# Kernel optimization log

Hardware: AMD Instinct MI355X
Metric: run time of the kernel (lower is better)

The kernel has to match this reference:

```python
import jax, jax.numpy as jnp
import numpy as np

# ---- model dims (match torch para_dict) ----
B, F1, F2, F_OUT = 16, 32, 64, 10
B0, B1, B2 = 32, 16, 8           # bandwidths: input / layer1 / layer2
M1, M2 = 2 * B1 - 1, 2 * B2 - 1  # padded spectral width over signed m
NUM_POINTS = 1
EPS = 1e-5

_LF = np.concatenate([[0.0], np.cumsum(np.log(np.arange(1.0, 200.0)))])  # _LF[i] = log(i!)

def _betas(b):
    return np.pi * (2.0 * np.arange(2 * b) + 1.0) / (4.0 * b)

def _quad_weights(b):
    # Driscoll-Healy quadrature weights on the 2b beta grid
    beta = _betas(b)
    k = np.arange(b)[:, None]
    s = np.sum(np.sin((2 * k + 1) * beta[None, :]) / (2 * k + 1), axis=0)
    return (2.0 / b) * np.sin(beta) * s

def _wig(l, m, n, betas):
    # small Wigner d^l_{m,n}(beta), vectorized over betas (float64)
    kmin, kmax = max(0, m - n), min(l + m, l - n)
    k = np.arange(kmin, kmax + 1)
    pref = 0.5 * (_LF[l + m] + _LF[l - m] + _LF[l + n] + _LF[l - n])
    coef = (-1.0) ** k * np.exp(pref - _LF[k] - _LF[l + m - k] - _LF[l - n - k] - _LF[n - m + k])
    cb, sb = np.cos(betas / 2)[:, None], np.sin(betas / 2)[:, None]
    return (coef * cb ** (2 * l + m - n - 2 * k) * sb ** (n - m + 2 * k)).sum(1)

def _build():
    b0g, b1g, b2g = _betas(B0), _betas(B1), _betas(B2)
    w0, w1q = _quad_weights(B0), _quad_weights(B1)
    d1f = np.zeros((B1, 2 * B0, M1))        # S2 forward: w_j * d^l_{m0}(beta_j)
    d1i = np.zeros((B1, 2 * B1, M1, M1))    # SO3 inverse at layer-1 grid, * (2l+1)
    d2f = np.zeros((B2, 2 * B1, M2, M2))    # SO3 forward at layer-1 grid, * w_j
    d2i = np.zeros((B2, 2 * B2, M2, M2))    # SO3 inverse at layer-2 grid, * (2l+1)
    mask1, mask2 = np.zeros((B1, M1)), np.zeros((B2, M2, M2))
    for l in range(B1):
        o = (B1 - 1) - l
        mask1[l, o:o + 2 * l + 1] = 1.0
        for m in range(-l, l + 1):
            d1f[l, :, o + m + l] = w0 * _wig(l, m, 0, b0g)
            for n in range(-l, l + 1):
                d1i[l, :, o + m + l, o + n + l] = (2 * l + 1) * _wig(l, m, n, b1g)
    for l in range(B2):
        o = (B2 - 1) - l
        mask2[l, o:o + 2 * l + 1, o:o + 2 * l + 1] = 1.0
        for m in range(-l, l + 1):
            for n in range(-l, l + 1):
                d2f[l, :, o + m + l, o + n + l] = w1q * _wig(l, m, n, b1g)
                d2i[l, :, o + m + l, o + n + l] = (2 * l + 1) * _wig(l, m, n, b2g)
    return d1f, d1i, d2f, d2i, mask1, mask2

_d1f, _d1i, _d2f, _d2i, _m1, _m2 = _build()
D1F = jnp.asarray(_d1f, jnp.float32)
D1I = jnp.asarray(_d1i, jnp.float32)
D2F = jnp.asarray(_d2f, jnp.float32)
D2I = jnp.asarray(_d2i, jnp.float32)
MASK1 = jnp.asarray(_m1, jnp.float32)
MASK2 = jnp.asarray(_m2, jnp.float32)
IDX1 = jnp.asarray(np.arange(-(B1 - 1), B1) % (2 * B0), jnp.int32)
IDXG1 = jnp.asarray(np.arange(-(B1 - 1), B1) % (2 * B1), jnp.int32)
IDX2 = jnp.asarray(np.arange(-(B2 - 1), B2) % (2 * B1), jnp.int32)
IDXG2 = jnp.asarray(np.arange(-(B2 - 1), B2) % (2 * B2), jnp.int32)

def _so3_ifft(yh, d_inv, idx, n):
    # yh: [B,F,L,M,M] SO3 spectrum -> signal [B,F,2b,2b,2b] on (beta, alpha, gamma)
    f = jnp.einsum('ljmn,bflmn->bfjmn', d_inv, yh)
    z = jnp.zeros(f.shape[:3] + (n, n), dtype=f.dtype)
    z = z.at[..., idx[:, None], idx[None, :]].set(f)
    return jnp.real(jnp.fft.ifft2(z, axes=(-2, -1))) * (n * n)

def _forward(x, w1r, w1i, w2r, w2i, conv3_w, conv3_b, bn_gamma, bn_beta, fc_w, fc_b):
    # ---- S2 convolution (b_in=B0 -> b_out=B1) ----
    xm = jnp.take(jnp.fft.fft(x, axis=-1), IDX1, axis=-1)      # alpha FFT, signed m  [B,1,2B0,M1]
    xh = jnp.einsum('ljm,bcjm->bclm', D1F, xm)                 # S2 FFT  [B,1,B1,M1]
    w1 = (w1r + 1j * w1i) * MASK1                              # [1,F1,B1,M1]
    yh1 = jnp.einsum('bclm,cfln->bflmn', xh, jnp.conj(w1))     # outer product -> SO3 spectrum
    r1 = jax.nn.relu(_so3_ifft(yh1, D1I, IDXG1, 2 * B1))       # [B,F1,2B1,2B1,2B1]
    # ---- SO3 convolution (b_in=B1 -> b_out=B2) ----
    xf2 = jnp.fft.fft2(r1, axes=(-2, -1))                      # over (alpha, gamma)
    xmn = xf2[..., IDX2[:, None], IDX2[None, :]]               # [B,F1,2B1,M2,M2]
    xh2 = jnp.einsum('ljmn,bcjmn->bclmn', D2F, xmn)            # SO3 FFT [B,F1,B2,M2,M2]
    w2 = (w2r + 1j * w2i) * MASK2                              # [F1,F2,B2,M2,M2]
    yh2 = jnp.einsum('bclmk,cflnk->bflmn', xh2, jnp.conj(w2))  # x_hat @ w_hat^H per l
    r2 = jax.nn.relu(_so3_ifft(yh2, D2I, IDXG2, 2 * B2))       # [B,F2,2B2,2B2,2B2]
    # ---- head: conv1d -> relu -> batchnorm(train) -> linear ----
    feat = r2[:, :, 0, 0, 0].reshape(B, 1, NUM_POINTS * F2)
    c3 = jax.lax.conv_general_dilated(feat, conv3_w, (1,), 'VALID',
                                      dimension_numbers=('NCH', 'OIH', 'NCH'))
    r3 = jax.nn.relu(c3 + conv3_b[None, :, None])              # [B,10,57]
    mu = jnp.mean(r3, axis=(0, 2), keepdims=True)
    var = jnp.mean((r3 - mu) ** 2, axis=(0, 2), keepdims=True)
    bn = bn_gamma[None, :, None] * (r3 - mu) * jax.lax.rsqrt(var + EPS) + bn_beta[None, :, None]
    return bn.reshape(B, -1) @ fc_w.T + fc_b

def setup_inputs():
    key = jax.random.key(0)
    ks = jax.random.split(key, 8)
    f = jnp.float32
    return {
        "x": jax.random.normal(ks[0], (B, 1, 2 * B0, 2 * B0), f),
        "w1r": 0.1 * jax.random.normal(ks[1], (1, F1, B1, M1), f),
        "w1i": 0.1 * jax.random.normal(ks[2], (1, F1, B1, M1), f),
        "w2r": 0.05 * jax.random.normal(ks[3], (F1, F2, B2, M2, M2), f),
        "w2i": 0.05 * jax.random.normal(ks[4], (F1, F2, B2, M2, M2), f),
        "conv3_w": 0.3 * jax.random.normal(ks[5], (10, 1, 8), f),
        "conv3_b": jnp.zeros((10,), f),
        "bn_gamma": jnp.ones((10,), f),
        "bn_beta": jnp.zeros((10,), f),
        "fc_w": 0.05 * jax.random.normal(ks[6], (F_OUT, 10 * (NUM_POINTS * F2 - 8 + 1)), f),
        "fc_b": jnp.zeros((F_OUT,), f),
    }

def reference(x, w1r, w1i, w2r, w2i, conv3_w, conv3_b, bn_gamma, bn_beta, fc_w, fc_b):
    return _forward(x, w1r, w1i, w2r, w2i, conv3_w, conv3_b, bn_gamma, bn_beta, fc_w, fc_b)
```

## Files before the change

kernel.cpp:

```cpp
#include <hip/hip_runtime.h>
#include <math.h>

#ifndef M_PI
#define M_PI 3.14159265358979323846
#endif

#define OFF_TRIG 708
#define OFF_D1F 900
#define OFF_D1I 32644
#define OFF_D2F 540548
#define OFF_S2  598148
#define OFF_XH  599948
#define OFF_XMN 615820
#define OFF_U   7988620
#define OFF_FEAT 9831820

static __device__ __forceinline__ int iabs_(int v) { return v < 0 ? -v : v; }

static __device__ __forceinline__ double powi_d(double x, int e) {
    double r = 1.0;
    while (e) { if (e & 1) r *= x; x *= x; e >>= 1; }
    return r;
}

__global__ __launch_bounds__(256) void k0a_tables(float* __restrict__ ws) {
    double* T = (double*)ws;
    int t = threadIdx.x;
    __shared__ double lg[64];
    if (t < 64) lg[t] = (t == 0) ? 0.0 : log((double)t);
    __syncthreads();
    if (t == 0) {
        double s = 0.0;
        for (int i = 0; i < 64; ++i) { s += lg[i]; T[i] = s; }
    }
    if (t < 64) {
        double beta = M_PI * (2.0 * t + 1.0) / 128.0;
        double s = 0.0;
        for (int k = 0; k < 32; ++k) s += sin((2.0 * k + 1.0) * beta) / (2.0 * k + 1.0);
        T[64 + t] = 2.0 / 32.0 * sin(beta) * s;
        T[160 + t] = cos(0.5 * beta);
        T[224 + t] = sin(0.5 * beta);
    }
    if (t >= 64 && t < 96) {
        int j = t - 64;
        double beta = M_PI * (2.0 * j + 1.0) / 64.0;
        double s = 0.0;
        for (int k = 0; k < 16; ++k) s += sin((2.0 * k + 1.0) * beta) / (2.0 * k + 1.0);
        T[128 + j] = 2.0 / 16.0 * sin(beta) * s;
        T[288 + j] = cos(0.5 * beta);
        T[320 + j] = sin(0.5 * beta);
    }
    if (t == 96) {
        T[352] = cos(M_PI / 64.0);
        T[353] = sin(M_PI / 64.0);
    }
    float2* F = (float2*)(ws + OFF_TRIG);
    if (t < 32) {
        double a = 2.0 * M_PI * (double)t / 32.0;
        F[t] = make_float2((float)cos(a), (float)sin(a));
    }
    if (t >= 128 && t < 192) {
        int i = t - 128;
        double a = 2.0 * M_PI * (double)i / 64.0;
        F[32 + i] = make_float2((float)cos(a), (float)sin(a));
    }
    for (int i = t; i < 1024; i += 256) ws[OFF_FEAT + i] = 0.f;
}

__device__ double wig_fast(int l, int m, int n, double cb, double sb, const double* LF) {
    int kmin = max(0, m - n), kmax = min(l + m, l - n);
    if (kmax < kmin) return 0.0;
    double lc = 0.5 * (LF[l + m] + LF[l - m] + LF[l + n] + LF[l - n])
              - LF[kmin] - LF[l + m - kmin] - LF[l - n - kmin] - LF[n - m + kmin];
    double t = exp(lc) * powi_d(cb, 2 * l + m - n - 2 * kmin)
                       * powi_d(sb, n - m + 2 * kmin);
    if (kmin & 1) t = -t;
    double ratio = (sb * sb) / (cb * cb);
    double s = t;
    for (int k = kmin; k < kmax; ++k) {
        t *= -(((double)(l + m - k) * (double)(l - n - k)) /
               ((double)(k + 1) * (double)(n - m + k + 1))) * ratio;
        s += t;
    }
    return s;
}

__global__ __launch_bounds__(256) void k0_consts(float* __restrict__ ws) {
    const double* T = (const double*)ws;
    __shared__ double LF[64];
    int tid = threadIdx.x;
    if (tid < 64) LF[tid] = T[tid];
    __syncthreads();
    int gid = blockIdx.x * 256 + tid;
    if (gid >= 599048) return;

    if (gid < 31744) {
        int mh = gid % 31, j = (gid / 31) % 64, l = gid / (31 * 64);
        int m = mh - 15;
        double v = 0.0;
        if (iabs_(m) <= l)
            v = T[64 + j] * wig_fast(l, m, 0, T[160 + j], T[224 + j], LF);
        ws[OFF_D1F + gid] = (float)v;
    } else if (gid < 539648) {
        int r = gid - 31744;
        int nh = r & 31;
        int l  = (r >> 5) & 15;
        int mh = (r >> 9) % 31;
        int j  = r / (512 * 31);
        int m = mh - 15, n = nh - 15;
        double v = 0.0;
        if (nh < 31 && iabs_(m) <= l && iabs_(n) <= l)
            v = (2.0 * l + 1.0) * wig_fast(l, m, n, T[288 + j], T[320 + j], LF);
        ws[OFF_D1I + r] = (float)v;
    } else if (gid < 597248) {
        int r = gid - 539648;
        int l = r & 7;
        int pq = (r >> 3) % 225;
        int j = r / 1800;
        int mh = pq / 15, nh = pq % 15;
        int m = mh - 7, n = nh - 7;
        double v = 0.0;
        if (iabs_(m) <= l && iabs_(n) <= l)
            v = T[128 + j] * wig_fast(l, m, n, T[288 + j], T[320 + j], LF);
        ws[OFF_D2F + r] = (float)v;
    } else {
        int r = gid - 597248;
        int nh = r % 15, mh = (r / 15) % 15, l = r / 225;
        int m = mh - 7, n = nh - 7;
        double v = 0.0;
        if (iabs_(m) <= l && iabs_(n) <= l)
            v = (2.0 * l + 1.0) * wig_fast(l, m, n, T[352], T[353], LF);
        ws[OFF_S2 + r] = (float)v;
    }
}

__global__ __launch_bounds__(256) void k1_xh(const float* __restrict__ x,
                                             const float* __restrict__ ws,
                                             float2* __restrict__ xh) {
    __shared__ float  xs[64 * 64];
    __shared__ float2 xm[64 * 8];
    __shared__ float2 cs64[64];
    int c = blockIdx.x, b = blockIdx.y, tid = threadIdx.x;
    int mh0 = c * 8;
    int cnt = min(8, 31 - mh0);
    for (int i = tid; i < 4096; i += 256) xs[i] = x[b * 4096 + i];
    if (tid < 64) cs64[tid] = ((const float2*)(ws + OFF_TRIG))[32 + tid];
    __syncthreads();
    for (int i = tid; i < 512; i += 256) {
        int j = i >> 3, mi = i & 7;
        if (mi < cnt) {
            int mu = mh0 + mi - 15;
            float re = 0.f, im = 0.f;
            for (int t = 0; t < 64; ++t) {
                float2 w = cs64[(mu * t) & 63];
                float xv = xs[j * 64 + t];
                re += xv * w.x;
                im -= xv * w.y;
            }
            xm[i] = make_float2(re, im);
        }
    }
    __syncthreads();
    const float* D1F = ws + OFF_D1F;
    if (tid < 128) {
        int l = tid >> 3, mi = tid & 7;
        if (mi < cnt) {
            int mh = mh0 + mi;
            float re = 0.f, im = 0.f;
            for (int j = 0; j < 64; ++j) {
                float d = D1F[(l * 64 + j) * 31 + mh];
                float2 v = xm[j * 8 + mi];
                re += d * v.x;
                im += d * v.y;
            }
            xh[b * 496 + l * 31 + mh] = make_float2(re, im);
        }
    }
}

__global__ __launch_bounds__(256) void k2_planes(const float* __restrict__ w1r,
                                                 const float* __restrict__ w1i,
                                                 const float* __restrict__ ws,
                                                 float2* __restrict__ xmn) {
    __shared__ char ar[16896];
    __shared__ float2 cs[32];
    float2* As  = (float2*)ar;
    float2* Wc  = (float2*)(ar + 4096);
    float2* f1  = (float2*)(ar + 8448);
    float2* fH  = (float2*)ar;
    float2* tls = (float2*)(ar + 4608);
    float*  ssb = (float*)(ar + 9216);
    float2* gg  = (float2*)ar;

    int j = blockIdx.x, f = blockIdx.y, b = blockIdx.z;
    int tid = threadIdx.x;
    const float2* xh = (const float2*)(ws + OFF_XH);

    if (tid < 32) cs[tid] = ((const float2*)(ws + OFF_TRIG))[tid];
    for (int i = tid; i < 496; i += 256) As[i] = xh[b * 496 + i];
    for (int i = tid; i < 512; i += 256) {
        int l = i >> 5, nh = i & 31;
        float mask = (nh < 31 && iabs_(nh - 15) <= l) ? 1.0f : 0.0f;
        int src = f * 496 + l * 31 + min(nh, 30);
        Wc[i] = make_float2(w1r[src] * mask, -w1i[src] * mask);
    }
    __syncthreads();
    {
        int mrow = tid >> 3;
        int nh0 = (tid & 7) * 4;
        if (mrow < 31) {
            int l0 = iabs_(mrow - 15);
            float2 a0 = {0,0}, a1 = {0,0}, a2 = {0,0}, a3 = {0,0};
            const float* Dbase = ws + OFF_D1I + ((j * 31 + mrow) * 16) * 32 + nh0;
            for (int l = l0; l < 16; ++l) {
                float2 a = As[l * 31 + mrow];
                float4 w01 = *(const float4*)(Wc + l * 32 + nh0);
                float4 w23 = *(const float4*)(Wc + l * 32 + nh0 + 2);
                float4 d = *(const float4*)(Dbase + l * 32);
                float t;
                t = a.x*w01.x - a.y*w01.y; a0.x += d.x*t;
                t = a.x*w01.y + a.y*w01.x; a0.y += d.x*t;
                t = a.x*w01.z - a.y*w01.w; a1.x += d.y*t;
                t = a.x*w01.w + a.y*w01.z; a1.y += d.y*t;
                t = a.x*w23.x - a.y*w23.y; a2.x += d.z*t;
                t = a.x*w23.y + a.y*w23.x; a2.y += d.z*t;
                t = a.x*w23.z - a.y*w23.w; a3.x += d.w*t;
                t = a.x*w23.w + a.y*w23.z; a3.y += d.w*t;
            }
            float2* fr = f1 + mrow * 34 + nh0;
            fr[0] = a0; fr[1] = a1; fr[2] = a2; fr[3] = a3;
        }
    }
    __syncthreads();
    for (int i = tid; i < 512; i += 256) {
        int mm = i >> 5, nh = i & 31;
        float2 v = make_float2(0.f, 0.f);
        if (nh < 31) {
            float2 a = f1[(mm + 15) * 34 + nh];
            float2 bb = f1[(15 - mm) * 34 + (30 - nh)];
            v = make_float2(0.5f * (a.x + bb.x), 0.5f * (a.y - bb.y));
        }
        fH[mm * 34 + nh] = v;
    }
    __syncthreads();
    if (tid < 128) {
        int mm = tid >> 3, v0 = tid & 7;
        const float2* frow = fH + mm * 34;
        float2 a0 = {0,0}, a1 = {0,0}, a2 = {0,0}, a3 = {0,0};
        for (int nb = 0; nb < 32; nb += 4) {
            float4 q01 = *(const float4*)(frow + nb);
            float4 q23 = *(const float4*)(frow + nb + 2);
            {
                float2 w = cs[((nb - 15) * v0) & 31];
                float px = q01.x*w.x - q01.y*w.y, py = q01.x*w.y + q01.y*w.x;
                a0.x += px; a0.y += py;  a1.x -= py; a1.y += px;
                a2.x -= px; a2.y -= py;  a3.x += py; a3.y -= px;
            }
            {
                float2 w = cs[((nb - 14) * v0) & 31];
                float px = q01.z*w.x - q01.w*w.y, py = q01.z*w.y + q01.w*w.x;
                a0.x += px; a0.y += py;  a1.x -= px; a1.y -= py;
                a2.x += px; a2.y += py;  a3.x -= px; a3.y -= py;
            }
            {
                float2 w = cs[((nb - 13) * v0) & 31];
                float px = q23.x*w.x - q23.y*w.y, py = q23.x*w.y + q23.y*w.x;
                a0.x += px; a0.y += py;  a1.x += py; a1.y -= px;
                a2.x -= px; a2.y -= py;  a3.x -= py; a3.y += px;
            }
            {
                float2 w = cs[((nb - 12) * v0) & 31];
                float px = q23.z*w.x - q23.w*w.y, py = q23.z*w.y + q23.w*w.x;
                a0.x += px; a0.y += py;  a1.x += px; a1.y += py;
                a2.x += px; a2.y += py;  a3.x += px; a3.y += py;
            }
        }
        float2* trow = tls + mm * 33;
        trow[v0] = a0; trow[v0 + 8] = a1; trow[v0 + 16] = a2; trow[v0 + 24] = a3;
    } else if (tid < 161) {
        tls[16 * 33 + (tid - 128)] = make_float2(0.f, 0.f);
    }
    __syncthreads();
    {
        int v = tid & 31, u0 = tid >> 5;
        float s0 = 0, s1 = 0, s2 = 0, s3 = 0;
        for (int mb = 0; mb < 4; ++mb) {
            int r1 = mb * 4 + 1;
            {
                float2 tv = tls[r1 * 33 + v];       float2 w = cs[(r1 * u0) & 31];
                float qx = tv.x*w.x - tv.y*w.y, qy = tv.x*w.y + tv.y*w.x;
                s0 += qx; s1 -= qy; s2 -= qx; s3 += qy;
            }
            {
                float2 tv = tls[(r1 + 1) * 33 + v]; float2 w = cs[((r1 + 1) * u0) & 31];
                float qx = tv.x*w.x - tv.y*w.y;
                s0 += qx; s1 -= qx; s2 += qx; s3 -= qx;
            }
            {
                float2 tv = tls[(r1 + 2) * 33 + v]; float2 w = cs[((r1 + 2) * u0) & 31];
                float qx = tv.x*w.x - tv.y*w.y, qy = tv.x*w.y + tv.y*w.x;
                s0 += qx; s1 += qy; s2 -= qx; s3 -= qy;
            }
            {
                float2 tv = tls[(r1 + 3) * 33 + v]; float2 w = cs[((r1 + 3) * u0) & 31];
                float qx = tv.x*w.x - tv.y*w.y;
                s0 += qx; s1 += qx; s2 += qx; s3 += qx;
            }
        }
        float t0x = tls[v].x;
        ssb[u0 * 33 + v]        = fmaxf(t0x + 2.f * s0, 0.f);
        ssb[(u0 + 8) * 33 + v]  = fmaxf(t0x + 2.f * s1, 0.f);
        ssb[(u0 + 16) * 33 + v] = fmaxf(t0x + 2.f * s2, 0.f);
        ssb[(u0 + 24) * 33 + v] = fmaxf(t0x + 2.f * s3, 0.f);
    }
    __syncthreads();
    {
        int u = tid >> 3, q = tid & 7;
        int qm = q & 3;
        float r1 = (qm == 0) ? 1.f : (qm == 2 ? -1.f : 0.f);
        float r2 = (qm & 1) ? -1.f : 1.f;
        float i1 = (qm == 1) ? -1.f : (qm == 3 ? 1.f : 0.f);
        float gx = 0.f, gy = 0.f;
        const float* srow = ssb + u * 33;
        for (int vb = 0; vb < 8; ++vb) {
            float s0 = srow[vb], s1 = srow[vb + 8], s2 = srow[vb + 16], s3 = srow[vb + 24];
            float zre = s0 + r1 * s1 + r2 * s2 + r1 * s3;
            float zim = i1 * (s1 - s3);
            float2 w = cs[(q * vb) & 31];
            gx += zre * w.x + zim * w.y;
            gy += zim * w.x - zre * w.y;
        }
        gg[u * 15 + 7 + q] = make_float2(gx, gy);
        if (q) gg[u * 15 + 7 - q] = make_float2(gx, -gy);
    }
    __syncthreads();
    if (tid < 113) {
        int ph, qh;
        if (tid < 105) { ph = 8 + tid / 15; qh = tid % 15; }
        else           { ph = 7; qh = 7 + (tid - 105); }
        int p = ph - 7;
        float hx = 0.f, hy = 0.f;
        for (int u = 0; u < 32; ++u) {
            float2 gv = gg[u * 15 + qh];
            float2 w = cs[(-(p * u)) & 31];
            hx += gv.x * w.x - gv.y * w.y;
            hy += gv.x * w.y + gv.y * w.x;
        }
        float2* outp = xmn + ((size_t)((b * 32 + f) * 32 + j)) * 225;
        outp[ph * 15 + qh] = make_float2(hx, hy);
        if (ph > 7 || qh > 7)
            outp[(14 - ph) * 15 + (14 - qh)] = make_float2(hx, -hy);
    }
}

__global__ __launch_bounds__(256) void k34_U(const float* __restrict__ ws,
                                             const float2* __restrict__ xmn,
                                             float2* __restrict__ U) {
    __shared__ float2 xh2s[1800];
    __shared__ float  S2s[1800];
    int bc = blockIdx.x, tid = threadIdx.x;

    for (int i = tid; i < 1800; i += 256) S2s[i] = ws[OFF_S2 + i];

    float2 acc[8];
#pragma unroll
    for (int l = 0; l < 8; ++l) acc[l] = make_float2(0.f, 0.f);
    if (tid < 225) {
        const float2* xp = xmn + (size_t)bc * 7200;
        const float4* dw = (const float4*)(ws + OFF_D2F);
        for (int j = 0; j < 32; ++j) {
            float2 xv = xp[j * 225 + tid];
            float4 dA = dw[(j * 225 + tid) * 2];
            float4 dB = dw[(j * 225 + tid) * 2 + 1];
            acc[0].x += dA.x * xv.x; acc[0].y += dA.x * xv.y;
            acc[1].x += dA.y * xv.x; acc[1].y += dA.y * xv.y;
            acc[2].x += dA.z * xv.x; acc[2].y += dA.z * xv.y;
            acc[3].x += dA.w * xv.x; acc[3].y += dA.w * xv.y;
            acc[4].x += dB.x * xv.x; acc[4].y += dB.x * xv.y;
            acc[5].x += dB.y * xv.x; acc[5].y += dB.y * xv.y;
            acc[6].x += dB.z * xv.x; acc[6].y += dB.z * xv.y;
            acc[7].x += dB.w * xv.x; acc[7].y += dB.w * xv.y;
        }
#pragma unroll
        for (int l = 0; l < 8; ++l) xh2s[l * 225 + tid] = acc[l];
    }
    __syncthreads();

    for (int idx = tid; idx < 1800; idx += 256) {
        int l = idx / 225;
        int rem = idx - l * 225;
        int n = rem / 15, k = rem - n * 15;
        float2 a = make_float2(0.f, 0.f);
        for (int m = 0; m < 15; ++m) {
            float s = S2s[(l * 15 + m) * 15 + n];
            float2 v = xh2s[l * 225 + m * 15 + k];
            a.x += s * v.x;
            a.y += s * v.y;
        }
        U[(size_t)bc * 1800 + idx] = a;
    }
}

__global__ __launch_bounds__(256) void k5_feat(const float* __restrict__ w2r,
                                               const float* __restrict__ w2i,
                                               const float2* __restrict__ U,
                                               float* __restrict__ feat) {
    __shared__ char ar[57600];
    float2* Us  = (float2*)ar;
    float2* Wsh = (float2*)(ar + 28800);
    int bx = blockIdx.x;
    int c = bx >> 5, l = (bx >> 2) & 7, fc = bx & 3;
    int tid = threadIdx.x;

    for (int i = tid; i < 3600; i += 256) {
        int b = i / 225, t = i - b * 225;
        Us[i] = U[(size_t)(b * 32 + c) * 1800 + l * 225 + t];
    }
    for (int i = tid; i < 3600; i += 256) {
        int f = fc * 16 + i / 225;
        int t = i % 225;
        int n = t / 15, k = t - n * 15;
        bool valid = (iabs_(n - 7) <= l) && (iabs_(k - 7) <= l);
        int wi = ((c * 64 + f) * 8 + l) * 225 + t;
        Wsh[i] = valid ? make_float2(w2r[wi], w2i[wi]) : make_float2(0.f, 0.f);
    }
    __syncthreads();
    int b = tid >> 4, fl = tid & 15;
    float accv = 0.f;
    const float2* up = Us + b * 225;
    const float2* wp = Wsh + fl * 225;
    for (int t = 0; t < 225; ++t)
        accv += up[t].x * wp[t].x + up[t].y * wp[t].y;
    atomicAdd(&feat[b * 64 + fc * 16 + fl], accv);
}

__global__ __launch_bounds__(640) void k6_head(const float* __restrict__ feat,
                                               const float* __restrict__ w3,
                                               const float* __restrict__ b3,
                                               const float* __restrict__ gamma,
                                               const float* __restrict__ beta,
                                               const float* __restrict__ fcw,
                                               const float* __restrict__ fcb,
                                               float* __restrict__ out) {
    __shared__ float fL[1024];
    __shared__ float w3L[80];
    __shared__ float b3L[10];
    __shared__ float r3[9120];
    __shared__ float scaleL[10], shiftL[10];
    int tid = threadIdx.x;
    for (int i = tid; i < 1024; i += 640) fL[i] = fmaxf(feat[i], 0.f);
    if (tid < 80) w3L[tid] = w3[tid];
    if (tid >= 80 && tid < 90) b3L[tid - 80] = b3[tid - 80];
    __syncthreads();
    for (int i = tid; i < 9120; i += 640) {
        int ch = i / 912;
        int r = i % 912;
        int b = r / 57, pos = r % 57;
        float acc = b3L[ch];
#pragma unroll
        for (int t = 0; t < 8; ++t) acc += fL[b * 64 + pos + t] * w3L[ch * 8 + t];
        r3[ch * 912 + r] = fmaxf(acc, 0.0f);
    }
    __syncthreads();
    int wave = tid >> 6, lane = tid & 63;
    if (wave < 10) {
        float s = 0.f, s2 = 0.f;
        for (int i = lane; i < 912; i += 64) {
            float v = r3[wave * 912 + i];
            s += v;
            s2 += v * v;
        }
        for (int off = 32; off > 0; off >>= 1) {
            s += __shfl_down(s, off);
            s2 += __shfl_down(s2, off);
        }
        if (lane == 0) {
            float mu = s / 912.0f;
            float var = s2 / 912.0f - mu * mu;
            float sc = gamma[wave] * rsqrtf(var + 1e-5f);
            scaleL[wave] = sc;
            shiftL[wave] = beta[wave] - mu * sc;
        }
    }
    __syncthreads();
    {
        int pair = tid >> 2, sub = tid & 3;
        int b = pair / 10, o = pair % 10;
        float acc = 0.f;
        for (int idx = sub; idx < 570; idx += 4) {
            int ch = idx / 57, pos = idx - ch * 57;
            acc += (r3[ch * 912 + b * 57 + pos] * scaleL[ch] + shiftL[ch])
                   * fcw[o * 570 + idx];
        }
        acc += __shfl_down(acc, 2);
        acc += __shfl_down(acc, 1);
        if (sub == 0) out[b * 10 + o] = acc + fcb[o];
    }
}

extern "C" void kernel_launch(void* const* d_in, const int* in_sizes, int n_in,
                              void* d_out, int out_size, void* d_ws, size_t ws_size,
                              hipStream_t stream) {
    const float* x   = (const float*)d_in[0];
    const float* w1r = (const float*)d_in[1];
    const float* w1i = (const float*)d_in[2];
    const float* w2r = (const float*)d_in[3];
    const float* w2i = (const float*)d_in[4];
    const float* c3w = (const float*)d_in[5];
    const float* c3b = (const float*)d_in[6];
    const float* bng = (const float*)d_in[7];
    const float* bnb = (const float*)d_in[8];
    const float* fcw = (const float*)d_in[9];
    const float* fcb = (const float*)d_in[10];
    float* ws = (float*)d_ws;
    float* out = (float*)d_out;

    hipLaunchKernelGGL(k0a_tables, dim3(1), dim3(256), 0, stream, ws);
    hipLaunchKernelGGL(k0_consts, dim3(2341), dim3(256), 0, stream, ws);
    hipLaunchKernelGGL(k1_xh, dim3(4, 16), dim3(256), 0, stream, x, ws,
                       (float2*)(ws + OFF_XH));
    hipLaunchKernelGGL(k2_planes, dim3(32, 32, 16), dim3(256), 0, stream, w1r, w1i, ws,
                       (float2*)(ws + OFF_XMN));
    hipLaunchKernelGGL(k34_U, dim3(512), dim3(256), 0, stream, ws,
                       (const float2*)(ws + OFF_XMN), (float2*)(ws + OFF_U));
    hipLaunchKernelGGL(k5_feat, dim3(1024), dim3(256), 0, stream, w2r, w2i,
                       (const float2*)(ws + OFF_U), ws + OFF_FEAT);
    hipLaunchKernelGGL(k6_head, dim3(1), dim3(640), 0, stream, ws + OFF_FEAT,
                       c3w, c3b, bng, bnb, fcw, fcb, out);
}
```

Baseline: 320.2 us.

## Replace atomic feature reduction with per-channel partials and radix-4 fold in k2

The feature contraction kernel is restructured so that each block handles one (batch, input channel) pair. It reads the needed w2 entries straight from global memory, skips masked entries, and writes per-channel partial sums. The head kernel then reduces these partials, which removes the atomics and the zero-init of the feature buffer. Separately, the inverse DFT over u in the planes kernel folds the four quarter-period samples first, cutting the inner loop from 32 to 8 complex multiplies. The new k5 reads w2 with strided, divergent global loads and has threads skip masked entries unevenly. It may also issue fewer blocks' worth of reuse than the previous shared-memory tiling.

```diff
diff --git a/kernel.cpp b/kernel.cpp
--- a/kernel.cpp
+++ b/kernel.cpp
@@ -13,7 +13,7 @@
 #define OFF_XH  599948
 #define OFF_XMN 615820
 #define OFF_U   7988620
-#define OFF_FEAT 9831820
+#define OFF_PART 9831820
 
 static __device__ __forceinline__ int iabs_(int v) { return v < 0 ? -v : v; }
 
@@ -64,7 +64,6 @@
         double a = 2.0 * M_PI * (double)i / 64.0;
         F[32 + i] = make_float2((float)cos(a), (float)sin(a));
     }
-    for (int i = t; i < 1024; i += 256) ws[OFF_FEAT + i] = 0.f;
 }
 
 __device__ double wig_fast(int l, int m, int n, double cb, double sb, const double* LF) {
@@ -339,12 +338,31 @@
         if (tid < 105) { ph = 8 + tid / 15; qh = tid % 15; }
         else           { ph = 7; qh = 7 + (tid - 105); }
         int p = ph - 7;
+        int pm = p & 3;
         float hx = 0.f, hy = 0.f;
-        for (int u = 0; u < 32; ++u) {
-            float2 gv = gg[u * 15 + qh];
-            float2 w = cs[(-(p * u)) & 31];
-            hx += gv.x * w.x - gv.y * w.y;
-            hy += gv.x * w.y + gv.y * w.x;
+        if ((pm & 1) == 0) {
+            float e = (pm == 0) ? 1.f : -1.f;
+            for (int u0 = 0; u0 < 8; ++u0) {
+                float2 g0 = gg[u0 * 15 + qh],      g1 = gg[(u0 + 8) * 15 + qh];
+                float2 g2 = gg[(u0 + 16) * 15 + qh], g3 = gg[(u0 + 24) * 15 + qh];
+                float zre = (g0.x + g2.x) + e * (g1.x + g3.x);
+                float zim = (g0.y + g2.y) + e * (g1.y + g3.y);
+                float2 w = cs[(-(p * u0)) & 31];
+                hx += zre * w.x - zim * w.y;
+                hy += zre * w.y + zim * w.x;
+            }
+        } else {
+            float s = (pm == 1) ? 1.f : -1.f;
+            for (int u0 = 0; u0 < 8; ++u0) {
+                float2 g0 = gg[u0 * 15 + qh],      g1 = gg[(u0 + 8) * 15 + qh];
+                float2 g2 = gg[(u0 + 16) * 15 + qh], g3 = gg[(u0 + 24) * 15 + qh];
+                float dx = g1.x - g3.x, dy = g1.y - g3.y;
+                float zre = (g0.x - g2.x) + s * dy;
+                float zim = (g0.y - g2.y) - s * dx;
+                float2 w = cs[(-(p * u0)) & 31];
+                hx += zre * w.x - zim * w.y;
+                hy += zre * w.y + zim * w.x;
+            }
         }
         float2* outp = xmn + ((size_t)((b * 32 + f) * 32 + j)) * 225;
         outp[ph * 15 + qh] = make_float2(hx, hy);
@@ -401,40 +419,33 @@
     }
 }
 
-__global__ __launch_bounds__(256) void k5_feat(const float* __restrict__ w2r,
+__global__ __launch_bounds__(256) void k5_part(const float* __restrict__ w2r,
                                                const float* __restrict__ w2i,
                                                const float2* __restrict__ U,
-                                               float* __restrict__ feat) {
-    __shared__ char ar[57600];
-    float2* Us  = (float2*)ar;
-    float2* Wsh = (float2*)(ar + 28800);
-    int bx = blockIdx.x;
-    int c = bx >> 5, l = (bx >> 2) & 7, fc = bx & 3;
+                                               float* __restrict__ part) {
+    __shared__ float2 Us[1800];
+    int b = blockIdx.x >> 5, c = blockIdx.x & 31;
     int tid = threadIdx.x;
-
-    for (int i = tid; i < 3600; i += 256) {
-        int b = i / 225, t = i - b * 225;
-        Us[i] = U[(size_t)(b * 32 + c) * 1800 + l * 225 + t];
-    }
-    for (int i = tid; i < 3600; i += 256) {
-        int f = fc * 16 + i / 225;
-        int t = i % 225;
-        int n = t / 15, k = t - n * 15;
-        bool valid = (iabs_(n - 7) <= l) && (iabs_(k - 7) <= l);
-        int wi = ((c * 64 + f) * 8 + l) * 225 + t;
-        Wsh[i] = valid ? make_float2(w2r[wi], w2i[wi]) : make_float2(0.f, 0.f);
-    }
-    __syncthreads();
-    int b = tid >> 4, fl = tid & 15;
-    float accv = 0.f;
-    const float2* up = Us + b * 225;
-    const float2* wp = Wsh + fl * 225;
-    for (int t = 0; t < 225; ++t)
-        accv += up[t].x * wp[t].x + up[t].y * wp[t].y;
-    atomicAdd(&feat[b * 64 + fc * 16 + fl], accv);
-}
-
-__global__ __launch_bounds__(640) void k6_head(const float* __restrict__ feat,
+    for (int i = tid; i < 1800; i += 256)
+        Us[i] = U[(size_t)(b * 32 + c) * 1800 + i];
+    __syncthreads();
+    int f = tid >> 2, sub = tid & 3;
+    float acc = 0.f;
+    for (int idx = sub; idx < 1800; idx += 4) {
+        int l = idx / 225;
+        int nk = idx - l * 225;
+        int n = nk / 15, k = nk - n * 15;
+        if (iabs_(n - 7) > l || iabs_(k - 7) > l) continue;
+        int wi = ((c * 64 + f) * 8 + l) * 225 + nk;
+        float2 u = Us[idx];
+        acc += u.x * w2r[wi] + u.y * w2i[wi];
+    }
+    acc += __shfl_down(acc, 2);
+    acc += __shfl_down(acc, 1);
+    if (sub == 0) part[(b * 64 + f) * 32 + c] = acc;
+}
+
+__global__ __launch_bounds__(640) void k6_head(const float* __restrict__ part,
                                                const float* __restrict__ w3,
                                                const float* __restrict__ b3,
                                                const float* __restrict__ gamma,
@@ -448,7 +459,13 @@
     __shared__ float r3[9120];
     __shared__ float scaleL[10], shiftL[10];
     int tid = threadIdx.x;
-    for (int i = tid; i < 1024; i += 640) fL[i] = fmaxf(feat[i], 0.f);
+    for (int i = tid; i < 1024; i += 640) {
+        const float* pp = part + i * 32;
+        float s = 0.f;
+#pragma unroll
+        for (int c = 0; c < 32; ++c) s += pp[c];
+        fL[i] = fmaxf(s, 0.f);
+    }
     if (tid < 80) w3L[tid] = w3[tid];
     if (tid >= 80 && tid < 90) b3L[tid - 80] = b3[tid - 80];
     __syncthreads();
@@ -523,8 +540,8 @@
                        (float2*)(ws + OFF_XMN));
     hipLaunchKernelGGL(k34_U, dim3(512), dim3(256), 0, stream, ws,
                        (const float2*)(ws + OFF_XMN), (float2*)(ws + OFF_U));
-    hipLaunchKernelGGL(k5_feat, dim3(1024), dim3(256), 0, stream, w2r, w2i,
-                       (const float2*)(ws + OFF_U), ws + OFF_FEAT);
-    hipLaunchKernelGGL(k6_head, dim3(1), dim3(640), 0, stream, ws + OFF_FEAT,
+    hipLaunchKernelGGL(k5_part, dim3(512), dim3(256), 0, stream, w2r, w2i,
+                       (const float2*)(ws + OFF_U), ws + OFF_PART);
+    hipLaunchKernelGGL(k6_head, dim3(1), dim3(640), 0, stream, ws + OFF_PART,
                        c3w, c3b, bng, bnb, fcw, fcb, out);
 }
```

Measured after the change: 382.1 us. 19.3% more time.
